# Kernel optimization log

Hardware: AMD Instinct MI355X
Metric: run time of the kernel (lower is better)

Reference implementation:

```python
import jax, jax.numpy as jnp
import numpy as np

B, L, D, V1, V2, V3 = 512, 48, 256, 512, 512, 64


def setup_inputs() -> dict:
    key = jax.random.key(0)
    ks = jax.random.split(key, 20)
    def w(k, shape, fan_in):
        return jax.random.normal(k, shape, dtype=jnp.float32) / np.sqrt(fan_in)
    inp = {
        'x1': jax.random.normal(ks[0], (B, L, V1), dtype=jnp.float32),
        'x2': jax.random.normal(ks[1], (B, L, V2), dtype=jnp.float32),
        's': jax.random.normal(ks[2], (B, V3), dtype=jnp.float32),
        'w_e1': w(ks[3], (D, V1), V1), 'b_e1': jnp.zeros((D,), jnp.float32),
        'w_e2': w(ks[4], (D, V2), V2), 'b_e2': jnp.zeros((D,), jnp.float32),
        'w_s': w(ks[5], (D, V3), V3), 'b_s': jnp.zeros((D,), jnp.float32),
        'w_x': w(ks[6], (1, D), D),                      # mlp_for_x, no bias
        'w_h': w(ks[7], (L, D), D), 'b_h': w(ks[8], (L,), D),  # mlp_for_hidden
        'w_ih': w(ks[9], (3 * D, D), D), 'w_hh': w(ks[10], (3 * D, D), D),
        'b_ih': w(ks[11], (3 * D,), D), 'b_hh': w(ks[12], (3 * D,), D),
        'w_out': w(ks[13], (1, D), D), 'b_out': jnp.zeros((1,), jnp.float32),
    }
    return inp


def _gru_cell(x, h, w_ih, w_hh, b_ih, b_hh):
    # torch GRUCell: gates ordered r, z, n
    gi = x @ w_ih.T + b_ih
    gh = h @ w_hh.T + b_hh
    i_r, i_z, i_n = jnp.split(gi, 3, axis=-1)
    h_r, h_z, h_n = jnp.split(gh, 3, axis=-1)
    r = jax.nn.sigmoid(i_r + h_r)
    z = jax.nn.sigmoid(i_z + h_z)
    n = jnp.tanh(i_n + r * h_n)
    return (1.0 - z) * n + z * h


def reference(x1, x2, s, w_e1, b_e1, w_e2, b_e2, w_s, b_s, w_x, w_h, b_h,
              w_ih, w_hh, b_ih, b_hh, w_out, b_out):
    x1e = jax.nn.relu(jnp.einsum('blv,dv->bld', x1, w_e1) + b_e1)
    x2e = jax.nn.relu(jnp.einsum('blv,dv->bld', x2, w_e2) + b_e2)
    se = s @ w_s.T + b_s                      # [B, D]
    x = x1e + x2e                             # [B, L, D]
    # prefix[:, i] = sum_{j < i} x2e[:, j, 0]  (the torch.where zero test)
    cums = jnp.cumsum(x2e[:, :, 0], axis=1)
    prefix = jnp.concatenate([jnp.zeros((B, 1), x.dtype), cums[:, :-1]], axis=1)  # [B, L]
    idx = jnp.arange(L)

    def step(h, inputs):
        i, pref = inputs                       # i: scalar step, pref: [B]
        le = (idx <= i).astype(x.dtype)        # keep timesteps 0..i (pad rest with 0)
        ip = x * le[None, :, None]             # input_padded [B, L, D]
        lt = (idx < i)
        cond = (pref == 0.0)[:, None]          # batches with zero history in ch0
        guid = jnp.where(idx[None, :] == i, 1.0,
                         jnp.where(cond & lt[None, :], 1.0, 0.0)).astype(x.dtype)  # [B, L]
        gi = ip * guid[:, :, None]
        t1 = jnp.einsum('bld,d->bl', gi, w_x[0]) + (h @ w_h.T + b_h)  # [B, L]
        a = jax.nn.softmax(t1, axis=1)
        ctx = jnp.einsum('bld,bl->bd', ip, a)
        h2 = _gru_cell(ctx, h, w_ih, w_hh, b_ih, b_hh)
        return h2, None

    h0 = jnp.zeros((B, D), x.dtype)
    hF, _ = jax.lax.scan(step, h0, (idx, prefix.T))
    y = jax.nn.sigmoid((hF + se) @ w_out.T + b_out)  # [B, 1]
    return y
```

## Files before the change

kernel.cpp:

```cpp
#include <hip/hip_runtime.h>
#include <stdint.h>

#define B_ 512
#define L_ 48
#define D_ 256

typedef __attribute__((ext_vector_type(8))) short bf16x8;
typedef __attribute__((ext_vector_type(4))) short bf16x4;
typedef __attribute__((ext_vector_type(4))) float f32x4;
typedef __attribute__((ext_vector_type(4))) int i32x4;

__device__ __forceinline__ short f2bf(float f) {
    union { float f; unsigned u; } v; v.f = f;
    unsigned u = v.u;
    unsigned r = (u + 0x7FFFu + ((u >> 16) & 1u)) >> 16;
    return (short)r;
}
__device__ __forceinline__ float bf2f(short s) {
    union { unsigned u; float f; } v; v.u = ((unsigned)(unsigned short)s) << 16;
    return v.f;
}

__global__ __launch_bounds__(256) void k_prep(const float* __restrict__ w_hh,
                                              const float* __restrict__ w_h,
                                              const float* __restrict__ w_ih,
                                              signed char* __restrict__ W1q,
                                              signed char* __restrict__ W2q,
                                              float* __restrict__ qA,
                                              float* __restrict__ qC) {
    int w = threadIdx.x >> 6, lane = threadIdx.x & 63;
    int R = blockIdx.x * 4 + w;
    if (R >= 1584) return;
    const float* src;
    signed char* dst;
    bool isA = (R < 816);
    if (R < 768)      { src = w_hh + (size_t)R * 256;         dst = W1q + (size_t)R * 256; }
    else if (R < 816) { src = w_h + (size_t)(R - 768) * 256;  dst = W1q + (size_t)R * 256; }
    else              { src = w_ih + (size_t)(R - 816) * 256; dst = W2q + (size_t)(R - 816) * 256; }
    float4 v = *(const float4*)(src + lane * 4);
    float m = fmaxf(fmaxf(fabsf(v.x), fabsf(v.y)), fmaxf(fabsf(v.z), fabsf(v.w)));
    #pragma unroll
    for (int o = 32; o; o >>= 1) m = fmaxf(m, __shfl_xor(m, o));
    float sc = (m > 0.f) ? 127.f / m : 0.f;
    int b0 = __float2int_rn(v.x * sc), b1 = __float2int_rn(v.y * sc);
    int b2 = __float2int_rn(v.z * sc), b3 = __float2int_rn(v.w * sc);
    unsigned word = (unsigned)(b0 & 255) | ((unsigned)(b1 & 255) << 8) |
                    ((unsigned)(b2 & 255) << 16) | ((unsigned)(b3 & 255) << 24);
    ((unsigned*)dst)[lane] = word;
    if (lane == 0) {
        if (isA) qA[R] = m / (127.f * 127.f);
        else     qC[R - 816] = m * 8.f / (127.f * 127.f);
    }
}

__device__ __forceinline__ void gemm_pass(const float* __restrict__ X,
                                          const float* __restrict__ W,
                                          short (*sA)[40], short (*sB)[40],
                                          int m0, int n0, int srow, int sseg,
                                          int mf, int nf, int row16, int kg,
                                          f32x4 (&acc)[2][4]) {
    for (int k0 = 0; k0 < 512; k0 += 32) {
        __syncthreads();
        {
            const float* src = X + (size_t)(m0 + srow) * 512 + k0 + sseg * 8;
            float4 p0 = *(const float4*)(src);
            float4 p1 = *(const float4*)(src + 4);
            bf16x8 v;
            v[0] = f2bf(p0.x); v[1] = f2bf(p0.y); v[2] = f2bf(p0.z); v[3] = f2bf(p0.w);
            v[4] = f2bf(p1.x); v[5] = f2bf(p1.y); v[6] = f2bf(p1.z); v[7] = f2bf(p1.w);
            *(bf16x8*)&sA[srow][sseg * 8] = v;
        }
        {
            const float* src = W + (size_t)(n0 + srow) * 512 + k0 + sseg * 8;
            float4 p0 = *(const float4*)(src);
            float4 p1 = *(const float4*)(src + 4);
            bf16x8 v;
            v[0] = f2bf(p0.x); v[1] = f2bf(p0.y); v[2] = f2bf(p0.z); v[3] = f2bf(p0.w);
            v[4] = f2bf(p1.x); v[5] = f2bf(p1.y); v[6] = f2bf(p1.z); v[7] = f2bf(p1.w);
            *(bf16x8*)&sB[srow][sseg * 8] = v;
        }
        __syncthreads();
        bf16x8 a0 = *(bf16x8*)&sA[(mf + 0) * 16 + row16][kg * 8];
        bf16x8 a1 = *(bf16x8*)&sA[(mf + 1) * 16 + row16][kg * 8];
        #pragma unroll
        for (int j = 0; j < 4; ++j) {
            bf16x8 bv = *(bf16x8*)&sB[(nf + j) * 16 + row16][kg * 8];
            acc[0][j] = __builtin_amdgcn_mfma_f32_16x16x32_bf16(a0, bv, acc[0][j], 0, 0, 0);
            acc[1][j] = __builtin_amdgcn_mfma_f32_16x16x32_bf16(a1, bv, acc[1][j], 0, 0, 0);
        }
    }
}

__global__ __launch_bounds__(512) void k_embed(const float* __restrict__ x1,
                                               const float* __restrict__ x2,
                                               const float* __restrict__ w_e1,
                                               const float* __restrict__ b_e1,
                                               const float* __restrict__ w_e2,
                                               const float* __restrict__ b_e2,
                                               short* __restrict__ xb) {
    __shared__ short sA[128][40];
    __shared__ short sB[128][40];
    int bid = blockIdx.x;
    int mt = bid >> 1, nt = bid & 1;
    int m0 = mt * 128, n0 = nt * 128;
    int tid = threadIdx.x;
    int lane = tid & 63, w = tid >> 6;
    int mf = (w & 3) * 2;
    int nf = (w >> 2) * 4;
    int row16 = lane & 15, kg = lane >> 4;
    int srow = tid >> 2, sseg = tid & 3;

    f32x4 acc[2][4], keep[2][4];
    #pragma unroll
    for (int a = 0; a < 2; ++a)
        #pragma unroll
        for (int j = 0; j < 4; ++j) { acc[a][j] = {0.f, 0.f, 0.f, 0.f}; }

    gemm_pass(x1, w_e1, sA, sB, m0, n0, srow, sseg, mf, nf, row16, kg, acc);
    #pragma unroll
    for (int a = 0; a < 2; ++a)
        #pragma unroll
        for (int j = 0; j < 4; ++j) { keep[a][j] = acc[a][j]; acc[a][j] = {0.f, 0.f, 0.f, 0.f}; }
    gemm_pass(x2, w_e2, sA, sB, m0, n0, srow, sseg, mf, nf, row16, kg, acc);

    #pragma unroll
    for (int a = 0; a < 2; ++a) {
        int mbase = m0 + (mf + a) * 16 + kg * 4;
        #pragma unroll
        for (int j = 0; j < 4; ++j) {
            int n = n0 + (nf + j) * 16 + row16;
            float be1 = b_e1[n], be2 = b_e2[n];
            #pragma unroll
            for (int e = 0; e < 4; ++e) {
                float v1 = fmaxf(keep[a][j][e] + be1, 0.f);
                float v2 = fmaxf(acc[a][j][e] + be2, 0.f);
                xb[(size_t)(mbase + e) * 256 + n] = f2bf(v1 + v2);
            }
        }
    }
}

__global__ __launch_bounds__(256) void k_quant(const short* __restrict__ xb,
                                               const float* __restrict__ w_x,
                                               signed char* __restrict__ xq,
                                               float* __restrict__ xs,
                                               float* __restrict__ xw) {
    int w = threadIdx.x >> 6, lane = threadIdx.x & 63;
    int row = blockIdx.x * 4 + w;
    const short* src = xb + (size_t)row * 256 + lane * 4;
    bf16x4 v = *(const bf16x4*)src;
    float f0 = bf2f(v.x), f1 = bf2f(v.y), f2 = bf2f(v.z), f3 = bf2f(v.w);
    float m = fmaxf(fmaxf(f0, f1), fmaxf(f2, f3));
    float t = f0 * w_x[lane * 4] + f1 * w_x[lane * 4 + 1] +
              f2 * w_x[lane * 4 + 2] + f3 * w_x[lane * 4 + 3];
    #pragma unroll
    for (int o = 32; o; o >>= 1) {
        m = fmaxf(m, __shfl_xor(m, o));
        t += __shfl_xor(t, o);
    }
    float sc = (m > 0.f) ? 127.f / m : 0.f;
    int b0 = __float2int_rn(f0 * sc), b1 = __float2int_rn(f1 * sc);
    int b2 = __float2int_rn(f2 * sc), b3 = __float2int_rn(f3 * sc);
    unsigned word = (unsigned)(b0 & 255) | ((unsigned)(b1 & 255) << 8) |
                    ((unsigned)(b2 & 255) << 16) | ((unsigned)(b3 & 255) << 24);
    ((unsigned*)xq)[(size_t)row * 64 + lane] = word;
    if (lane == 0) { xs[row] = m / 127.f; xw[row] = t; }
}

__global__ __launch_bounds__(256) void k_aux(const float* __restrict__ x2,
                                             const float* __restrict__ w_e2,
                                             const float* __restrict__ b_e2,
                                             float* __restrict__ c0) {
    int w = threadIdx.x >> 6, lane = threadIdx.x & 63;
    int m = blockIdx.x * 4 + w;
    const float* xr = x2 + (size_t)m * 512 + lane * 8;
    const float* wr = w_e2 + lane * 8;
    float s = 0.f;
    #pragma unroll
    for (int q = 0; q < 8; ++q) s += xr[q] * wr[q];
    #pragma unroll
    for (int o = 32; o; o >>= 1) s += __shfl_xor(s, o);
    if (lane == 0) c0[m] = fmaxf(s + b_e2[0], 0.f);
}

__global__ __launch_bounds__(256) void k_aux2(const float* __restrict__ c0,
                                              const float* __restrict__ s_in,
                                              const float* __restrict__ w_s,
                                              const float* __restrict__ b_s,
                                              unsigned long long* __restrict__ condbits,
                                              float* __restrict__ se) {
    __shared__ float sS[64];
    int b = blockIdx.x;
    int t = threadIdx.x;
    if (t < 64) sS[t] = s_in[b * 64 + t];
    __syncthreads();
    float acc = b_s[t];
    const float* wr = w_s + t * 64;
    #pragma unroll 8
    for (int kk = 0; kk < 64; ++kk) acc += sS[kk] * wr[kk];
    se[(size_t)b * 256 + t] = acc;
    if (t == 0) {
        unsigned long long bits = 0;
        bool run = true;
        const float* cr = c0 + (size_t)b * 48;
        for (int i = 0; i < 48; ++i) {
            if (run) bits |= (1ull << i);
            run = run && (cr[i] == 0.0f);
        }
        condbits[b] = bits;
    }
}

__device__ __forceinline__ void mfma4r(const i32x4 (&a)[4], const i32x4 (&b)[4], i32x4& acc) {
    #pragma unroll
    for (int s = 0; s < 4; ++s)
        acc = __builtin_amdgcn_mfma_i32_16x16x64_i8(a[s], b[s], acc, 0, 0, 0);
}

__global__ __launch_bounds__(512, 1) void k_scan(const signed char* __restrict__ W1q,
                                                 const signed char* __restrict__ W2q,
                                                 const float* __restrict__ qAg,
                                                 const float* __restrict__ qCg,
                                                 const float* __restrict__ b_hh,
                                                 const float* __restrict__ b_h,
                                                 const float* __restrict__ b_ih,
                                                 const signed char* __restrict__ xq,
                                                 const float* __restrict__ xs,
                                                 const float* __restrict__ xw,
                                                 const unsigned long long* __restrict__ condbits,
                                                 const float* __restrict__ se,
                                                 const float* __restrict__ w_out,
                                                 const float* __restrict__ b_out,
                                                 float* __restrict__ out) {
    __shared__ signed char lWc[8][3][4096];
    __shared__ signed char lWs[3][4096];
    __shared__ signed char lXq[2 * 48 * 256];
    __shared__ signed char lH8[16][272];
    __shared__ signed char lX8[16][272];
    __shared__ float lS[16][52];
    __shared__ float lTw[8][49];
    __shared__ float lXW[2][48], lXS[2][48];
    __shared__ float lbA[816], lqA[816], lbC[768], lqC[768];
    __shared__ float lRed[8][2];
    __shared__ unsigned long long lC[2];

    const int tid = threadIdx.x;
    const int w = tid >> 6, lane = tid & 63;
    const int row16 = lane & 15, kg = lane >> 4;
    const int b0 = blockIdx.x * 2;
    const int g1 = 8 + w;
    const int c0 = w * 16 + row16, c1 = g1 * 16 + row16;
    const int swz = (row16 & 7) << 4;
    const float CS = 127.f / 8.f;
    const int mb = w >> 2;
    const int dimb = ((w & 3) << 6) + lane;

    for (int t = tid; t < 816; t += 512) {
        lbA[t] = (t < 768) ? b_hh[t] : b_h[t - 768];
        lqA[t] = qAg[t];
    }
    for (int t = tid; t < 768; t += 512) { lbC[t] = b_ih[t]; lqC[t] = qCg[t]; }
    if (tid < 96) {
        int m = tid / 48, j = tid - m * 48;
        lXW[m][j] = xw[(size_t)(b0 + m) * 48 + j];
        lXS[m][j] = xs[(size_t)(b0 + m) * 48 + j];
    }
    if (tid < 2) lC[tid] = condbits[b0 + tid];
    for (int t = tid; t < 1088; t += 512) {
        ((int*)lH8)[t] = 0;
        ((int*)lX8)[t] = 0;
    }
    {
        const int4* src = (const int4*)(xq + (size_t)b0 * 48 * 256);
        int4* dst = (int4*)lXq;
        #pragma unroll
        for (int t = 0; t < 3; ++t) dst[tid + t * 512] = src[tid + t * 512];
    }

    const int fro = row16 * 256 + kg * 16;
    i32x4 wa0[3][4], wa1[3][4], wc0[3][4];
    #pragma unroll
    for (int t = 0; t < 3; ++t) {
        const signed char* p0 = W1q + (size_t)(t * 16 + w) * 4096 + fro;
        const signed char* p1 = W1q + (size_t)(t * 16 + g1) * 4096 + fro;
        const signed char* p2 = W2q + (size_t)(t * 16 + w) * 4096 + fro;
        #pragma unroll
        for (int s = 0; s < 4; ++s) {
            wa0[t][s] = *(const i32x4*)(p0 + s * 64);
            wa1[t][s] = *(const i32x4*)(p1 + s * 64);
            wc0[t][s] = *(const i32x4*)(p2 + s * 64);
        }
    }
    #pragma unroll
    for (int t = 0; t < 3; ++t) {
        const signed char* src = W2q + (size_t)(t * 16 + g1) * 4096 + fro;
        signed char* dst = &lWc[w][t][row16 * 256];
        #pragma unroll
        for (int s = 0; s < 4; ++s)
            *(i32x4*)(dst + ((kg * 16 + s * 64) ^ swz)) = *(const i32x4*)(src + s * 64);
    }
    if (w < 3) {
        const signed char* src = W1q + (size_t)(48 + w) * 4096 + fro;
        signed char* dst = &lWs[w][row16 * 256];
        #pragma unroll
        for (int s = 0; s < 4; ++s)
            *(i32x4*)(dst + ((kg * 16 + s * 64) ^ swz)) = *(const i32x4*)(src + s * 64);
    }
    __syncthreads();

    const signed char* xl = lXq + mb * 12288 + dimb;

    float h0[2] = {0.f, 0.f};
    float h1[2] = {0.f, 0.f};

    for (int i = 0; i < 48; ++i) {
        i32x4 av[4];
        #pragma unroll
        for (int s = 0; s < 4; ++s) av[s] = *(const i32x4*)(&lH8[row16][0] + kg * 16 + s * 64);
        if (w < 3) {
            i32x4 scv = {0,0,0,0};
            #pragma unroll
            for (int s = 0; s < 4; ++s) {
                i32x4 b = *(const i32x4*)(&lWs[w][row16 * 256] + ((kg * 16 + s * 64) ^ swz));
                scv = __builtin_amdgcn_mfma_i32_16x16x64_i8(av[s], b, scv, 0, 0, 0);
            }
            const int n = 768 + w * 16 + row16;
            const float q = lqA[n], bb = lbA[n];
            #pragma unroll
            for (int e = 0; e < 2; ++e) lS[kg * 4 + e][w * 16 + row16] = (float)scv[e] * q + bb;
        }
        i32x4 aR0 = {0,0,0,0}, aZ0 = {0,0,0,0}, aN0 = {0,0,0,0};
        i32x4 aR1 = {0,0,0,0}, aZ1 = {0,0,0,0}, aN1 = {0,0,0,0};
        mfma4r(av, wa0[0], aR0); mfma4r(av, wa0[1], aZ0); mfma4r(av, wa0[2], aN0);
        mfma4r(av, wa1[0], aR1); mfma4r(av, wa1[1], aZ1); mfma4r(av, wa1[2], aN1);
        __syncthreads();

        {
            float val = -3.0e38f;
            if (lane < 48) {
                val = lS[mb][lane];
                bool cb = (lC[mb] >> i) & 1ull;
                if (lane == i) val += lXW[mb][i];
                else if (cb && lane < i) val += lXW[mb][lane];
            }
            float mx = val;
            #pragma unroll
            for (int o = 32; o; o >>= 1) mx = fmaxf(mx, __shfl_xor(mx, o));
            float ex = (lane < 48) ? __expf(val - mx) : 0.f;
            float sm = ex;
            #pragma unroll
            for (int o = 32; o; o >>= 1) sm += __shfl_xor(sm, o);
            if (lane < 48) lTw[w][lane] = (ex / sm) * lXS[mb][lane];
        }
        {
            const float* tw = lTw[w];
            float acc = 0.f;
            #pragma unroll 4
            for (int j = 0; j <= i; ++j)
                acc += tw[j] * (float)xl[j * 256];
            lX8[mb][dimb] = (signed char)__float2int_rn(fminf(fmaxf(acc * CS, -127.f), 127.f));
        }
        __syncthreads();

        i32x4 cv[4];
        #pragma unroll
        for (int s = 0; s < 4; ++s) cv[s] = *(const i32x4*)(&lX8[row16][0] + kg * 16 + s * 64);
        {
            i32x4 cr = {0,0,0,0}, cz = {0,0,0,0}, cn = {0,0,0,0};
            mfma4r(cv, wc0[0], cr); mfma4r(cv, wc0[1], cz); mfma4r(cv, wc0[2], cn);
            #pragma unroll
            for (int e = 0; e < 2; ++e) {
                float gr = (float)aR0[e] * lqA[c0]       + lbA[c0]       + (float)cr[e] * lqC[c0]       + lbC[c0];
                float gz = (float)aZ0[e] * lqA[256 + c0] + lbA[256 + c0] + (float)cz[e] * lqC[256 + c0] + lbC[256 + c0];
                float gh = (float)aN0[e] * lqA[512 + c0] + lbA[512 + c0];
                float gn = (float)cn[e] * lqC[512 + c0]  + lbC[512 + c0];
                float r = 1.f / (1.f + __expf(-gr));
                float z = 1.f / (1.f + __expf(-gz));
                float nn = 1.f - 2.f / (__expf(2.f * (gn + r * gh)) + 1.f);
                float hp = (1.f - z) * nn + z * h0[e];
                h0[e] = hp;
                if (kg == 0)
                    lH8[e][c0] = (signed char)__float2int_rn(fminf(fmaxf(hp, -1.f), 1.f) * 127.f);
            }
        }
        {
            i32x4 cr = {0,0,0,0}, cz = {0,0,0,0}, cn = {0,0,0,0};
            #pragma unroll
            for (int s = 0; s < 4; ++s) {
                int off = (kg * 16 + s * 64) ^ swz;
                i32x4 br = *(const i32x4*)(&lWc[w][0][row16 * 256] + off);
                i32x4 bz = *(const i32x4*)(&lWc[w][1][row16 * 256] + off);
                i32x4 bn = *(const i32x4*)(&lWc[w][2][row16 * 256] + off);
                cr = __builtin_amdgcn_mfma_i32_16x16x64_i8(cv[s], br, cr, 0, 0, 0);
                cz = __builtin_amdgcn_mfma_i32_16x16x64_i8(cv[s], bz, cz, 0, 0, 0);
                cn = __builtin_amdgcn_mfma_i32_16x16x64_i8(cv[s], bn, cn, 0, 0, 0);
            }
            #pragma unroll
            for (int e = 0; e < 2; ++e) {
                float gr = (float)aR1[e] * lqA[c1]       + lbA[c1]       + (float)cr[e] * lqC[c1]       + lbC[c1];
                float gz = (float)aZ1[e] * lqA[256 + c1] + lbA[256 + c1] + (float)cz[e] * lqC[256 + c1] + lbC[256 + c1];
                float gh = (float)aN1[e] * lqA[512 + c1] + lbA[512 + c1];
                float gn = (float)cn[e] * lqC[512 + c1]  + lbC[512 + c1];
                float r = 1.f / (1.f + __expf(-gr));
                float z = 1.f / (1.f + __expf(-gz));
                float nn = 1.f - 2.f / (__expf(2.f * (gn + r * gh)) + 1.f);
                float hp = (1.f - z) * nn + z * h1[e];
                h1[e] = hp;
                if (kg == 0)
                    lH8[e][c1] = (signed char)__float2int_rn(fminf(fmaxf(hp, -1.f), 1.f) * 127.f);
            }
        }
        __syncthreads();
    }

    if (kg == 0) {
        float p[2];
        #pragma unroll
        for (int e = 0; e < 2; ++e) {
            int b = b0 + e;
            p[e] = (h0[e] + se[(size_t)b * 256 + c0]) * w_out[c0]
                 + (h1[e] + se[(size_t)b * 256 + c1]) * w_out[c1];
        }
        #pragma unroll
        for (int o = 1; o < 16; o <<= 1) {
            #pragma unroll
            for (int e = 0; e < 2; ++e) p[e] += __shfl_xor(p[e], o);
        }
        if (row16 == 0) {
            #pragma unroll
            for (int e = 0; e < 2; ++e) lRed[w][e] = p[e];
        }
    }
    __syncthreads();
    if (tid < 2) {
        float sum = 0.f;
        #pragma unroll
        for (int q = 0; q < 8; ++q) sum += lRed[q][tid];
        out[b0 + tid] = 1.f / (1.f + __expf(-(sum + b_out[0])));
    }
}

extern "C" void kernel_launch(void* const* d_in, const int* in_sizes, int n_in,
                              void* d_out, int out_size, void* d_ws, size_t ws_size,
                              hipStream_t stream) {
    const float* x1   = (const float*)d_in[0];
    const float* x2   = (const float*)d_in[1];
    const float* s    = (const float*)d_in[2];
    const float* w_e1 = (const float*)d_in[3];
    const float* b_e1 = (const float*)d_in[4];
    const float* w_e2 = (const float*)d_in[5];
    const float* b_e2 = (const float*)d_in[6];
    const float* w_s  = (const float*)d_in[7];
    const float* b_s  = (const float*)d_in[8];
    const float* w_x  = (const float*)d_in[9];
    const float* w_h  = (const float*)d_in[10];
    const float* b_h  = (const float*)d_in[11];
    const float* w_ih = (const float*)d_in[12];
    const float* w_hh = (const float*)d_in[13];
    const float* b_ih = (const float*)d_in[14];
    const float* b_hh = (const float*)d_in[15];
    const float* w_out = (const float*)d_in[16];
    const float* b_out = (const float*)d_in[17];
    float* out = (float*)d_out;

    char* ws = (char*)d_ws;
    size_t off = 0;
    auto alloc = [&](size_t bytes) -> void* {
        void* p = ws + off;
        off = (off + bytes + 255) & ~(size_t)255;
        return p;
    };
    short* xb = (short*)alloc((size_t)B_ * L_ * D_ * 2);
    signed char* xq = (signed char*)alloc((size_t)B_ * L_ * D_);
    float* xs = (float*)alloc((size_t)B_ * L_ * 4);
    signed char* W1q = (signed char*)alloc(896 * 256);
    signed char* W2q = (signed char*)alloc(768 * 256);
    float* qA = (float*)alloc(816 * 4);
    float* qC = (float*)alloc(768 * 4);
    float* c0 = (float*)alloc((size_t)B_ * L_ * 4);
    float* xw = (float*)alloc((size_t)B_ * L_ * 4);
    unsigned long long* cb = (unsigned long long*)alloc(B_ * 8);
    float* se = (float*)alloc((size_t)B_ * D_ * 4);

    hipLaunchKernelGGL(k_prep, dim3(396), dim3(256), 0, stream,
                       w_hh, w_h, w_ih, W1q, W2q, qA, qC);
    hipLaunchKernelGGL(k_embed, dim3(384), dim3(512), 0, stream,
                       x1, x2, w_e1, b_e1, w_e2, b_e2, xb);
    hipLaunchKernelGGL(k_quant, dim3(6144), dim3(256), 0, stream,
                       xb, w_x, xq, xs, xw);
    hipLaunchKernelGGL(k_aux, dim3(6144), dim3(256), 0, stream,
                       x2, w_e2, b_e2, c0);
    hipLaunchKernelGGL(k_aux2, dim3(512), dim3(256), 0, stream,
                       c0, s, w_s, b_s, cb, se);
    hipLaunchKernelGGL(k_scan, dim3(256), dim3(512), 0, stream,
                       W1q, W2q, qA, qC, b_hh, b_h, b_ih, xq, xs, xw, cb, se,
                       w_out, b_out, out);
}
```

Measured before the change: 241.6 us.

## Fuse channel-0 x2 embedding into embed GEMM and keep scan per-row scalars in registers

The channel-0 ReLU projection of x2 is now accumulated in fp32 inside the embed GEMM's x2 load loop (only for n-tile 0 blocks), removing the separate k_aux kernel, its launch and its second full read of x2. In the scan kernel, per-batch xw/xs values and the cond bitmask are loaded once into registers instead of shared memory. The score buffer shrinks to two rows written by one lane group. The fused dot adds some ALU and load work and a branch to half the embed blocks.

Measured after the change: 235.7 us. -2.5%, faster.

```diff
diff --git a/kernel.cpp b/kernel.cpp
--- a/kernel.cpp
+++ b/kernel.cpp
@@ -91,13 +91,59 @@
     }
 }
 
+__device__ __forceinline__ void gemm_pass_c0(const float* __restrict__ X,
+                                             const float* __restrict__ W,
+                                             const float* __restrict__ we2r0,
+                                             bool doC0, float& c0acc,
+                                             short (*sA)[40], short (*sB)[40],
+                                             int m0, int n0, int srow, int sseg,
+                                             int mf, int nf, int row16, int kg,
+                                             f32x4 (&acc)[2][4]) {
+    for (int k0 = 0; k0 < 512; k0 += 32) {
+        __syncthreads();
+        {
+            const float* src = X + (size_t)(m0 + srow) * 512 + k0 + sseg * 8;
+            float4 p0 = *(const float4*)(src);
+            float4 p1 = *(const float4*)(src + 4);
+            if (doC0) {
+                const float* wr = we2r0 + k0 + sseg * 8;
+                c0acc += p0.x * wr[0] + p0.y * wr[1] + p0.z * wr[2] + p0.w * wr[3]
+                       + p1.x * wr[4] + p1.y * wr[5] + p1.z * wr[6] + p1.w * wr[7];
+            }
+            bf16x8 v;
+            v[0] = f2bf(p0.x); v[1] = f2bf(p0.y); v[2] = f2bf(p0.z); v[3] = f2bf(p0.w);
+            v[4] = f2bf(p1.x); v[5] = f2bf(p1.y); v[6] = f2bf(p1.z); v[7] = f2bf(p1.w);
+            *(bf16x8*)&sA[srow][sseg * 8] = v;
+        }
+        {
+            const float* src = W + (size_t)(n0 + srow) * 512 + k0 + sseg * 8;
+            float4 p0 = *(const float4*)(src);
+            float4 p1 = *(const float4*)(src + 4);
+            bf16x8 v;
+            v[0] = f2bf(p0.x); v[1] = f2bf(p0.y); v[2] = f2bf(p0.z); v[3] = f2bf(p0.w);
+            v[4] = f2bf(p1.x); v[5] = f2bf(p1.y); v[6] = f2bf(p1.z); v[7] = f2bf(p1.w);
+            *(bf16x8*)&sB[srow][sseg * 8] = v;
+        }
+        __syncthreads();
+        bf16x8 a0 = *(bf16x8*)&sA[(mf + 0) * 16 + row16][kg * 8];
+        bf16x8 a1 = *(bf16x8*)&sA[(mf + 1) * 16 + row16][kg * 8];
+        #pragma unroll
+        for (int j = 0; j < 4; ++j) {
+            bf16x8 bv = *(bf16x8*)&sB[(nf + j) * 16 + row16][kg * 8];
+            acc[0][j] = __builtin_amdgcn_mfma_f32_16x16x32_bf16(a0, bv, acc[0][j], 0, 0, 0);
+            acc[1][j] = __builtin_amdgcn_mfma_f32_16x16x32_bf16(a1, bv, acc[1][j], 0, 0, 0);
+        }
+    }
+}
+
 __global__ __launch_bounds__(512) void k_embed(const float* __restrict__ x1,
                                                const float* __restrict__ x2,
                                                const float* __restrict__ w_e1,
                                                const float* __restrict__ b_e1,
                                                const float* __restrict__ w_e2,
                                                const float* __restrict__ b_e2,
-                                               short* __restrict__ xb) {
+                                               short* __restrict__ xb,
+                                               float* __restrict__ c0) {
     __shared__ short sA[128][40];
     __shared__ short sB[128][40];
     int bid = blockIdx.x;
@@ -121,7 +167,17 @@
     for (int a = 0; a < 2; ++a)
         #pragma unroll
         for (int j = 0; j < 4; ++j) { keep[a][j] = acc[a][j]; acc[a][j] = {0.f, 0.f, 0.f, 0.f}; }
-    gemm_pass(x2, w_e2, sA, sB, m0, n0, srow, sseg, mf, nf, row16, kg, acc);
+
+    float c0acc = 0.f;
+    const bool doC0 = (nt == 0);
+    gemm_pass_c0(x2, w_e2, w_e2, doC0, c0acc, sA, sB, m0, n0, srow, sseg, mf, nf, row16, kg, acc);
+
+    if (doC0) {
+        float t = c0acc;
+        t += __shfl_xor(t, 1);
+        t += __shfl_xor(t, 2);
+        if (sseg == 0) c0[m0 + srow] = fmaxf(t + b_e2[0], 0.f);
+    }
 
     #pragma unroll
     for (int a = 0; a < 2; ++a) {
@@ -165,22 +221,6 @@
                     ((unsigned)(b2 & 255) << 16) | ((unsigned)(b3 & 255) << 24);
     ((unsigned*)xq)[(size_t)row * 64 + lane] = word;
     if (lane == 0) { xs[row] = m / 127.f; xw[row] = t; }
-}
-
-__global__ __launch_bounds__(256) void k_aux(const float* __restrict__ x2,
-                                             const float* __restrict__ w_e2,
-                                             const float* __restrict__ b_e2,
-                                             float* __restrict__ c0) {
-    int w = threadIdx.x >> 6, lane = threadIdx.x & 63;
-    int m = blockIdx.x * 4 + w;
-    const float* xr = x2 + (size_t)m * 512 + lane * 8;
-    const float* wr = w_e2 + lane * 8;
-    float s = 0.f;
-    #pragma unroll
-    for (int q = 0; q < 8; ++q) s += xr[q] * wr[q];
-    #pragma unroll
-    for (int o = 32; o; o >>= 1) s += __shfl_xor(s, o);
-    if (lane == 0) c0[m] = fmaxf(s + b_e2[0], 0.f);
 }
 
 __global__ __launch_bounds__(256) void k_aux2(const float* __restrict__ c0,
@@ -237,12 +277,10 @@
     __shared__ signed char lXq[2 * 48 * 256];
     __shared__ signed char lH8[16][272];
     __shared__ signed char lX8[16][272];
-    __shared__ float lS[16][52];
+    __shared__ float lS[2][52];
     __shared__ float lTw[8][49];
-    __shared__ float lXW[2][48], lXS[2][48];
     __shared__ float lbA[816], lqA[816], lbC[768], lqC[768];
     __shared__ float lRed[8][2];
-    __shared__ unsigned long long lC[2];
 
     const int tid = threadIdx.x;
     const int w = tid >> 6, lane = tid & 63;
@@ -260,12 +298,6 @@
         lqA[t] = qAg[t];
     }
     for (int t = tid; t < 768; t += 512) { lbC[t] = b_ih[t]; lqC[t] = qCg[t]; }
-    if (tid < 96) {
-        int m = tid / 48, j = tid - m * 48;
-        lXW[m][j] = xw[(size_t)(b0 + m) * 48 + j];
-        lXS[m][j] = xs[(size_t)(b0 + m) * 48 + j];
-    }
-    if (tid < 2) lC[tid] = condbits[b0 + tid];
     for (int t = tid; t < 1088; t += 512) {
         ((int*)lH8)[t] = 0;
         ((int*)lX8)[t] = 0;
@@ -276,6 +308,10 @@
         #pragma unroll
         for (int t = 0; t < 3; ++t) dst[tid + t * 512] = src[tid + t * 512];
     }
+
+    const float xwv = (lane < 48) ? xw[(size_t)(b0 + mb) * 48 + lane] : 0.f;
+    const float xsv = (lane < 48) ? xs[(size_t)(b0 + mb) * 48 + lane] : 0.f;
+    const unsigned long long cbits = condbits[b0 + mb];
 
     const int fro = row16 * 256 + kg * 16;
     i32x4 wa0[3][4], wa1[3][4], wc0[3][4];
@@ -326,8 +362,10 @@
             }
             const int n = 768 + w * 16 + row16;
             const float q = lqA[n], bb = lbA[n];
-            #pragma unroll
-            for (int e = 0; e < 2; ++e) lS[kg * 4 + e][w * 16 + row16] = (float)scv[e] * q + bb;
+            if (kg == 0) {
+                #pragma unroll
+                for (int e = 0; e < 2; ++e) lS[e][w * 16 + row16] = (float)scv[e] * q + bb;
+            }
         }
         i32x4 aR0 = {0,0,0,0}, aZ0 = {0,0,0,0}, aN0 = {0,0,0,0};
         i32x4 aR1 = {0,0,0,0}, aZ1 = {0,0,0,0}, aN1 = {0,0,0,0};
@@ -339,9 +377,8 @@
             float val = -3.0e38f;
             if (lane < 48) {
                 val = lS[mb][lane];
-                bool cb = (lC[mb] >> i) & 1ull;
-                if (lane == i) val += lXW[mb][i];
-                else if (cb && lane < i) val += lXW[mb][lane];
+                bool cb = (cbits >> i) & 1ull;
+                if (lane == i || (cb && lane < i)) val += xwv;
             }
             float mx = val;
             #pragma unroll
@@ -350,7 +387,7 @@
             float sm = ex;
             #pragma unroll
             for (int o = 32; o; o >>= 1) sm += __shfl_xor(sm, o);
-            if (lane < 48) lTw[w][lane] = (ex / sm) * lXS[mb][lane];
+            if (lane < 48) lTw[w][lane] = (ex / sm) * xsv;
         }
         {
             const float* tw = lTw[w];
@@ -485,11 +522,9 @@
     hipLaunchKernelGGL(k_prep, dim3(396), dim3(256), 0, stream,
                        w_hh, w_h, w_ih, W1q, W2q, qA, qC);
     hipLaunchKernelGGL(k_embed, dim3(384), dim3(512), 0, stream,
-                       x1, x2, w_e1, b_e1, w_e2, b_e2, xb);
+                       x1, x2, w_e1, b_e1, w_e2, b_e2, xb, c0);
     hipLaunchKernelGGL(k_quant, dim3(6144), dim3(256), 0, stream,
                        xb, w_x, xq, xs, xw);
-    hipLaunchKernelGGL(k_aux, dim3(6144), dim3(256), 0, stream,
-                       x2, w_e2, b_e2, c0);
     hipLaunchKernelGGL(k_aux2, dim3(512), dim3(256), 0, stream,
                        c0, s, w_s, b_s, cb, se);
     hipLaunchKernelGGL(k_scan, dim3(256), dim3(512), 0, stream,
```
